# Performance work log

Hardware: AMD Instinct MI355X
Metric: run time of the kernel (lower is better)

The kernel has to match this reference:

```python
import jax, jax.numpy as jnp
import numpy as np

N = 96                      # n_size: neurons per row/column
WAVELENGTH = 1.55e-6        # telecom wavelength (m)
PITCH = 1.55e-6             # neuron spacing = wavelength (m)
Z_SRC = 0.0                 # z of this layer
Z_NEXT = 1e-5               # z of next layer


def setup_inputs() -> dict:
    key = jax.random.key(0)
    k1, k2 = jax.random.split(key)
    x = jax.random.normal(k1, (N, N), dtype=jnp.float32)
    weights = jax.random.normal(k2, (N, N), dtype=jnp.float32)
    coords = (jnp.arange(N, dtype=jnp.float32) - (N - 1) / 2.0) * PITCH
    return {"x": x, "weights": weights, "x_coords": coords, "y_coords": coords}


def reference(x, weights, x_coords, y_coords):
    # Transmission matrix: unit-amplitude, phase = weights  ->  e^{j*w}
    # (weights mod 2*pi gives the same complex value, so exp(1j*w) is exact)
    modes = (jnp.exp(1j * weights) * x).reshape(-1)          # (M,) complex64, M = N*N

    # Neuron grid positions (same x/y grid on both planes, differing only in z)
    xx, yy = jnp.meshgrid(x_coords, y_coords, indexing="ij")
    px = xx.reshape(-1)                                       # (M,)
    py = yy.reshape(-1)                                       # (M,)
    dz = Z_NEXT - Z_SRC

    # Pairwise source->detector distances, (M, M)
    dx = px[:, None] - px[None, :]
    dy = py[:, None] - py[None, :]
    r = jnp.sqrt(dx * dx + dy * dy + dz * dz)

    # First Rayleigh-Sommerfeld diffraction kernel:
    #   w(r) = (dz / r^2) * (1/(2*pi*r) + 1/(j*lambda)) * exp(j*2*pi*r/lambda) * dA
    k = 2.0 * jnp.pi / WAVELENGTH
    g = (dz / (r * r)) * (1.0 / (2.0 * jnp.pi * r) + 1.0 / (1j * WAVELENGTH)) \
        * jnp.exp(1j * k * r)                                 # (M, M) complex64

    dA = PITCH * PITCH
    out = jnp.einsum("i,ij->j", modes, g) * dA                # (M,)
    return out.reshape(N, N)
```

## Files before the change

kernel.cpp:

```cpp
#include <hip/hip_runtime.h>
#include <math.h>


#define NN 96
#define M (NN*NN)
#define GH 191
#define GWG 192
#define GW2 200
#define MW2 104

__device__ float2 g_G[GH * GWG];
__device__ float2 g_modes[M];

__global__ __launch_bounds__(256) void precompute_kernel(
    const float* __restrict__ x, const float* __restrict__ w,
    const float* __restrict__ xc, const float* __restrict__ yc) {
  const double DZ     = 1e-5;
  const double LAMBDA = 1.55e-6;
  const double PI     = 3.14159265358979323846;
  const double K      = 2.0 * PI / LAMBDA;
  const double DA     = 1.55e-6 * 1.55e-6;

  int idx = blockIdx.x * 256 + threadIdx.x;
  if (idx < GH * GH) {
    int u = idx / GH - (NN - 1);
    int v = idx % GH - (NN - 1);
    int au = u < 0 ? -u : u;
    int av = v < 0 ? -v : v;
    double dx = (double)xc[au] - (double)xc[0];
    double dy = (double)yc[av] - (double)yc[0];
    double r2 = dx * dx + dy * dy + DZ * DZ;
    double r  = sqrt(r2);
    double amp = DZ / r2 * DA;
    double A = amp / (2.0 * PI * r);
    double B = amp / LAMBDA;
    double s, c;
    sincos(K * r, &s, &c);
    g_G[(u + NN - 1) * GWG + (v + NN - 1)] =
        make_float2((float)(A * c + B * s), (float)(A * s - B * c));
  } else if (idx < GH * GH + M) {
    int i = idx - GH * GH;
    float s, c;
    __sincosf(0.0f, &s, &c);
    sincosf(w[i], &s, &c);
    float xv = x[i];
    g_modes[i] = make_float2(c * xv, s * xv);
  }
}

__global__ __launch_bounds__(192) void conv_kernel(float* __restrict__ out,
                                                   int interleaved) {
  int c  = blockIdx.x;
  int a0 = blockIdx.y * 8;
  int t  = threadIdx.x;

  __shared__ float2 s_modes[8 * MW2];
  __shared__ float2 s_G[8 * GW2 + 8];
  __shared__ float2 s_red[8 * NN];

  {
    float4* dst = (float4*)s_modes;
    const float4* src = (const float4*)(g_modes + a0 * NN);
    #pragma unroll
    for (int k = 0; k < 2; ++k) {
      int idx = k * 192 + t;
      int row = idx / 48, col = idx % 48;
      ((float4*)(s_modes + row * MW2))[col] = src[row * 48 + col];
      (void)dst;
    }
  }
  #pragma unroll
  for (int k = 0; k < 4; ++k) {
    int idx = k * 192 + t;
    int row = idx / 96, col = idx % 96;
    const float4* src = (const float4*)(g_G + (a0 + row - c + (NN - 1)) * GWG);
    ((float4*)(s_G + row * GW2))[col] = src[col];
  }
  __syncthreads();

  int q = t % 24;
  int h = t / 24;
  int base = 92 - 4 * q;
  const float4* Grow = (const float4*)(s_G + h * GW2);
  const float4* Mrow = (const float4*)(s_modes + h * MW2);
  int gb = base >> 1;

  float4 g0 = Grow[gb];
  float4 g1 = Grow[gb + 1];
  float4 g2 = Grow[gb + 2];
  float2 a0c = {0.f, 0.f}, a1c = {0.f, 0.f}, a2c = {0.f, 0.f}, a3c = {0.f, 0.f};

#define CFMA(acc, mr, mi, gr, gi)                 \
  acc.x = fmaf(mr, gr, acc.x);                    \
  acc.x = fmaf(-(mi), gi, acc.x);                 \
  acc.y = fmaf(mr, gi, acc.y);                    \
  acc.y = fmaf(mi, gr, acc.y)

  for (int b = 0; b < NN; b += 2) {
    float4 mm = Mrow[b >> 1];
    CFMA(a0c, mm.x, mm.y, g1.z, g1.w);
    CFMA(a0c, mm.z, mm.w, g2.x, g2.y);
    CFMA(a1c, mm.x, mm.y, g1.x, g1.y);
    CFMA(a1c, mm.z, mm.w, g1.z, g1.w);
    CFMA(a2c, mm.x, mm.y, g0.z, g0.w);
    CFMA(a2c, mm.z, mm.w, g1.x, g1.y);
    CFMA(a3c, mm.x, mm.y, g0.x, g0.y);
    CFMA(a3c, mm.z, mm.w, g0.z, g0.w);
    g0 = g1;
    g1 = g2;
    g2 = Grow[gb + 3 + (b >> 1)];
  }
#undef CFMA

  int dbase = 4 * q;
  s_red[h * NN + dbase + 0] = a0c;
  s_red[h * NN + dbase + 1] = a1c;
  s_red[h * NN + dbase + 2] = a2c;
  s_red[h * NN + dbase + 3] = a3c;
  __syncthreads();

  if (t < NN) {
    float re = 0.f, im = 0.f;
    #pragma unroll
    for (int hh = 0; hh < 8; ++hh) {
      re += s_red[hh * NN + t].x;
      im += s_red[hh * NN + t].y;
    }
    int j = c * NN + t;
    if (interleaved) {
      atomicAdd(out + 2 * j,     re);
      atomicAdd(out + 2 * j + 1, im);
    } else {
      atomicAdd(out + j, re);
    }
  }
}

extern "C" void kernel_launch(void* const* d_in, const int* in_sizes, int n_in,
                              void* d_out, int out_size, void* d_ws, size_t ws_size,
                              hipStream_t stream) {
  const float* x  = (const float*)d_in[0];
  const float* w  = (const float*)d_in[1];
  const float* xc = (const float*)d_in[2];
  const float* yc = (const float*)d_in[3];
  float* out = (float*)d_out;

  hipMemsetAsync(d_out, 0, (size_t)out_size * sizeof(float), stream);

  int total = GH * GH + M;
  precompute_kernel<<<(total + 255) / 256, 256, 0, stream>>>(x, w, xc, yc);

  int interleaved = (out_size >= 2 * M) ? 1 : 0;
  conv_kernel<<<dim3(NN, 12), 192, 0, stream>>>(out, interleaved);
}
```

Measured before the change: 76.83 us.

## Fuse precompute and convolution into one kernel with grid-wide barriers

Merges the kernel-table/mode precompute and the convolution into a single launch, using atomic-counter spin barriers across all 1152 blocks to order the phases. Partial sums per chunk are written to workspace and reduced deterministically by chunk-0 blocks, which replaces the output memset and float atomics with a workspace counter memset. It also cheapens the phase evaluation by doing range reduction in double and then a fast float sincos. The spin barriers assume every block is co-resident; if they are not, the kernel deadlocks, and the reduced-precision sincos changes numerical accuracy.

```diff
diff --git a/kernel.cpp b/kernel.cpp
--- a/kernel.cpp
+++ b/kernel.cpp
@@ -8,66 +8,74 @@
 #define GWG 192
 #define GW2 200
 #define MW2 104
+#define NBLK (NN*12)
 
 __device__ float2 g_G[GH * GWG];
 __device__ float2 g_modes[M];
 
-__global__ __launch_bounds__(256) void precompute_kernel(
+__global__ __launch_bounds__(192, 4) void fused_kernel(
     const float* __restrict__ x, const float* __restrict__ w,
-    const float* __restrict__ xc, const float* __restrict__ yc) {
-  const double DZ     = 1e-5;
-  const double LAMBDA = 1.55e-6;
-  const double PI     = 3.14159265358979323846;
-  const double K      = 2.0 * PI / LAMBDA;
-  const double DA     = 1.55e-6 * 1.55e-6;
+    const float* __restrict__ xc, const float* __restrict__ yc,
+    float* __restrict__ out, int interleaved,
+    int* __restrict__ cnt, float2* __restrict__ part) {
 
-  int idx = blockIdx.x * 256 + threadIdx.x;
-  if (idx < GH * GH) {
-    int u = idx / GH - (NN - 1);
-    int v = idx % GH - (NN - 1);
-    int au = u < 0 ? -u : u;
-    int av = v < 0 ? -v : v;
-    double dx = (double)xc[au] - (double)xc[0];
-    double dy = (double)yc[av] - (double)yc[0];
+  const int c     = blockIdx.x;
+  const int chunk = blockIdx.y;
+  const int a0    = chunk * 8;
+  const int t     = threadIdx.x;
+  const int gid   = (chunk * NN + c) * 192 + t;
+
+  const double DZ = 1e-5, LAMBDA = 1.55e-6;
+  const double TWO_PI     = 6.283185307179586476925;
+  const double INV_TWO_PI = 0.15915494309189533577;
+  const double K  = TWO_PI / LAMBDA;
+  const double DA = LAMBDA * LAMBDA;
+
+  if (gid < GH * GH) {
+    int u = gid / GH - (NN - 1);
+    int v = gid % GH - (NN - 1);
+    double dx = (double)xc[u < 0 ? -u : u] - (double)xc[0];
+    double dy = (double)yc[v < 0 ? -v : v] - (double)yc[0];
     double r2 = dx * dx + dy * dy + DZ * DZ;
     double r  = sqrt(r2);
-    double amp = DZ / r2 * DA;
-    double A = amp / (2.0 * PI * r);
+    double invr2 = 1.0 / r2;
+    double amp = DZ * DA * invr2;
+    double A = amp * INV_TWO_PI * (r * invr2);
     double B = amp / LAMBDA;
-    double s, c;
-    sincos(K * r, &s, &c);
+    double ph = K * r;
+    double nred = rint(ph * INV_TWO_PI);
+    float red = (float)fma(-nred, TWO_PI, ph);
+    float s, cs;
+    __sincosf(red, &s, &cs);
     g_G[(u + NN - 1) * GWG + (v + NN - 1)] =
-        make_float2((float)(A * c + B * s), (float)(A * s - B * c));
-  } else if (idx < GH * GH + M) {
-    int i = idx - GH * GH;
-    float s, c;
-    __sincosf(0.0f, &s, &c);
-    sincosf(w[i], &s, &c);
+        make_float2((float)(A * cs + B * s), (float)(A * s - B * cs));
+  } else if (gid < GH * GH + M) {
+    int i = gid - GH * GH;
+    float s, cs;
+    sincosf(w[i], &s, &cs);
     float xv = x[i];
-    g_modes[i] = make_float2(c * xv, s * xv);
+    g_modes[i] = make_float2(cs * xv, s * xv);
   }
-}
 
-__global__ __launch_bounds__(192) void conv_kernel(float* __restrict__ out,
-                                                   int interleaved) {
-  int c  = blockIdx.x;
-  int a0 = blockIdx.y * 8;
-  int t  = threadIdx.x;
+  __threadfence();
+  __syncthreads();
+  if (t == 0) {
+    __hip_atomic_fetch_add(cnt, 1, __ATOMIC_RELEASE, __HIP_MEMORY_SCOPE_AGENT);
+    while (__hip_atomic_load(cnt, __ATOMIC_ACQUIRE, __HIP_MEMORY_SCOPE_AGENT) < NBLK)
+      __builtin_amdgcn_s_sleep(2);
+  }
+  __syncthreads();
 
   __shared__ float2 s_modes[8 * MW2];
   __shared__ float2 s_G[8 * GW2 + 8];
   __shared__ float2 s_red[8 * NN];
 
-  {
-    float4* dst = (float4*)s_modes;
-    const float4* src = (const float4*)(g_modes + a0 * NN);
-    #pragma unroll
-    for (int k = 0; k < 2; ++k) {
-      int idx = k * 192 + t;
-      int row = idx / 48, col = idx % 48;
-      ((float4*)(s_modes + row * MW2))[col] = src[row * 48 + col];
-      (void)dst;
-    }
+  #pragma unroll
+  for (int k = 0; k < 2; ++k) {
+    int idx = k * 192 + t;
+    int row = idx / 48, col = idx % 48;
+    const float4* src = (const float4*)(g_modes + (a0 + row) * NN);
+    ((float4*)(s_modes + row * MW2))[col] = src[col];
   }
   #pragma unroll
   for (int k = 0; k < 4; ++k) {
@@ -126,12 +134,35 @@
       re += s_red[hh * NN + t].x;
       im += s_red[hh * NN + t].y;
     }
+    part[chunk * M + c * NN + t] = make_float2(re, im);
+  }
+
+  __threadfence();
+  __syncthreads();
+  if (t == 0)
+    __hip_atomic_fetch_add(cnt + 1, 1, __ATOMIC_RELEASE, __HIP_MEMORY_SCOPE_AGENT);
+  if (chunk != 0) return;
+
+  if (t == 0) {
+    while (__hip_atomic_load(cnt + 1, __ATOMIC_ACQUIRE, __HIP_MEMORY_SCOPE_AGENT) < NBLK)
+      __builtin_amdgcn_s_sleep(2);
+  }
+  __syncthreads();
+
+  if (t < NN) {
+    float re = 0.f, im = 0.f;
+    #pragma unroll
+    for (int k = 0; k < 12; ++k) {
+      float2 p = part[k * M + c * NN + t];
+      re += p.x;
+      im += p.y;
+    }
     int j = c * NN + t;
     if (interleaved) {
-      atomicAdd(out + 2 * j,     re);
-      atomicAdd(out + 2 * j + 1, im);
+      out[2 * j]     = re;
+      out[2 * j + 1] = im;
     } else {
-      atomicAdd(out + j, re);
+      out[j] = re;
     }
   }
 }
@@ -145,11 +176,12 @@
   const float* yc = (const float*)d_in[3];
   float* out = (float*)d_out;
 
-  hipMemsetAsync(d_out, 0, (size_t)out_size * sizeof(float), stream);
+  int*    cnt  = (int*)d_ws;
+  float2* part = (float2*)((char*)d_ws + 256);
 
-  int total = GH * GH + M;
-  precompute_kernel<<<(total + 255) / 256, 256, 0, stream>>>(x, w, xc, yc);
+  hipMemsetAsync(d_ws, 0, 256, stream);
 
   int interleaved = (out_size >= 2 * M) ? 1 : 0;
-  conv_kernel<<<dim3(NN, 12), 192, 0, stream>>>(out, interleaved);
+  fused_kernel<<<dim3(NN, 12), 192, 0, stream>>>(x, w, xc, yc, out,
+                                                 interleaved, cnt, part);
 }
```

After: 272.8 us. 3.55x slower.
